# Performance work log

Measured on AMD Instinct MI355X. Metric: run time of the kernel, lower is better.

The kernel has to match this reference:

```python
import jax, jax.numpy as jnp
import numpy as np

B, T, D = 2, 2048, 2048
H, HD = 16, 128          # n_heads, head_dim = d_out // n_heads
DC, DR = 512, 64         # latent dim d_c, rope dim d_R


def _rope(x):
    """RoPE over last dim (even), positions along axis -2. x: [..., T, Dr]."""
    half = x.shape[-1] // 2
    t = x.shape[-2]
    inv_freq = 1.0 / (10000.0 ** (jnp.arange(half, dtype=jnp.float32) / half))
    freqs = jnp.arange(t, dtype=jnp.float32)[:, None] * inv_freq[None, :]  # [T, half]
    sin, cos = jnp.sin(freqs), jnp.cos(freqs)
    x1, x2 = x[..., :half], x[..., half:]
    # stack pairs on a new last axis then flatten -> interleaved layout,
    # matching torch.stack((...), dim=-1) followed by implicit flatten
    rot = jnp.stack([x1 * cos - x2 * sin, x1 * sin + x2 * cos], axis=-1)
    return rot.reshape(x.shape[:-1] + (2 * half,))


def setup_inputs() -> dict:
    key = jax.random.key(0)
    ks = jax.random.split(key, 10)
    s = 0.02  # init scale
    return {
        "x":     jax.random.normal(ks[0], (B, T, D), dtype=jnp.float32),
        "W_DKV": jax.random.normal(ks[1], (D, DC), dtype=jnp.float32) * s,
        "W_DQ":  jax.random.normal(ks[2], (D, DC), dtype=jnp.float32) * s,
        "W_UK":  jax.random.normal(ks[3], (DC, D), dtype=jnp.float32) * s,
        "W_UV":  jax.random.normal(ks[4], (DC, D), dtype=jnp.float32) * s,
        "W_UQ":  jax.random.normal(ks[5], (DC, D), dtype=jnp.float32) * s,
        "W_KR":  jax.random.normal(ks[6], (D, DR), dtype=jnp.float32) * s,
        "W_QR":  jax.random.normal(ks[7], (DC, H * DR), dtype=jnp.float32) * s,
        "W_O":   jax.random.normal(ks[8], (D, D), dtype=jnp.float32) * s,
        "b_O":   jax.random.normal(ks[9], (D,), dtype=jnp.float32) * s,
    }


def reference(x, W_DKV, W_DQ, W_UK, W_UV, W_UQ, W_KR, W_QR, W_O, b_O):
    b, t, d = x.shape
    # latent KV compression and up-projection
    c_kv = x @ W_DKV                                        # [B,T,d_c]
    K = (c_kv @ W_UK).reshape(b, t, H, HD).transpose(0, 2, 1, 3)  # [B,H,T,hd]
    V = (c_kv @ W_UV).reshape(b, t, H, HD).transpose(0, 2, 1, 3)
    # latent Q compression and up-projection
    c_q = x @ W_DQ                                          # [B,T,d_c]
    Q = (c_q @ W_UQ).reshape(b, t, H, HD).transpose(0, 2, 1, 3)
    # decoupled RoPE channels: shared rotary key per token, per-head rotary query
    k_R = _rope(x @ W_KR)[:, None, :, :]                    # [B,1,T,d_R]
    k_R = jnp.broadcast_to(k_R, (b, H, t, DR))
    q_R = (c_q @ W_QR).reshape(b, t, H, DR).transpose(0, 2, 1, 3)  # [B,H,T,d_R]
    q_R = _rope(q_R)
    # concat content + rotary channels
    Kf = jnp.concatenate([K, k_R], axis=-1)                 # [B,H,T,hd+d_R]
    Qf = jnp.concatenate([Q, q_R], axis=-1)
    scale = 1.0 / jnp.sqrt(jnp.float32(HD + DR))
    scores = jnp.einsum('bhqd,bhkd->bhqk', Qf, Kf) * scale  # [B,H,T,T]
    attn = jax.nn.softmax(scores, axis=-1)                  # dropout is identity (p=0 / eval)
    ctx = jnp.einsum('bhqk,bhkd->bhqd', attn, V)            # [B,H,T,hd]
    ctx = ctx.transpose(0, 2, 1, 3).reshape(b, t, d)
    return ctx @ W_O + b_O
```

## Files before the change

### kernel.cpp

```cpp
#include <hip/hip_runtime.h>
#include <hip/hip_bf16.h>

typedef __attribute__((ext_vector_type(8))) short short8;
typedef __attribute__((ext_vector_type(4))) short s4_t;
typedef __attribute__((ext_vector_type(4))) float f32x4;
typedef __attribute__((ext_vector_type(16))) float f32x16;
typedef __attribute__((ext_vector_type(2))) unsigned uint2v;
typedef __hip_bfloat16 bf16;

#define NB 2
#define NT 2048
#define NDIM 2048
#define NH 16
#define NHD 128
#define NDC 512
#define NDR 64

__device__ __forceinline__ void gl_lds16(const bf16* g, bf16* l){
  __builtin_amdgcn_global_load_lds(
      (const __attribute__((address_space(1))) void*)(const void*)g,
      (__attribute__((address_space(3))) void*)(void*)l, 16, 0, 0);
}

__global__ __launch_bounds__(256) void cvt_kernel(const float* __restrict__ src, bf16* __restrict__ dst){
  int i = (blockIdx.x*256 + threadIdx.x)*4;
  float4 v = *(const float4*)(src + i);
  dst[i+0] = __float2bfloat16(v.x);
  dst[i+1] = __float2bfloat16(v.y);
  dst[i+2] = __float2bfloat16(v.z);
  dst[i+3] = __float2bfloat16(v.w);
}

struct TAll {
  const float* src[8];
  bf16* dst[8];
  int K[8];
  int N[8];
  int cum[9];
};
__global__ __launch_bounds__(256) void tconv_all(TAll a){
  __shared__ float tile[32][33];
  int bid = blockIdx.x;
  int i = 0;
  #pragma unroll
  for (int j=0;j<8;j++) if (bid >= a.cum[j+1]) i = j+1;
  const float* W = a.src[i];
  bf16* Wt = a.dst[i];
  int K = a.K[i], N = a.N[i];
  int tl = bid - a.cum[i];
  int ntx = N >> 5;
  int n0 = (tl % ntx)*32, k0 = (tl / ntx)*32;
  int tx = threadIdx.x & 31, ty = threadIdx.x >> 5;
  #pragma unroll
  for (int j=0;j<32;j+=8) tile[ty+j][tx] = W[(size_t)(k0+ty+j)*N + n0 + tx];
  __syncthreads();
  #pragma unroll
  for (int j=0;j<32;j+=8) Wt[(size_t)(n0+ty+j)*K + k0 + tx] = __float2bfloat16(tile[tx][ty+j]);
}

template<int MODE>
__global__ __launch_bounds__(256,3) void gemm_bt(const bf16* __restrict__ A,
    const bf16* __restrict__ Bt, bf16* __restrict__ C, float* __restrict__ Cf,
    const float* __restrict__ bias, int M, int N, int K, int lda, int Tq, int Dpad, float mult)
{
  __shared__ bf16 As[128*64];
  __shared__ bf16 Bs[128*64];
  const int m0 = blockIdx.x*128, n0 = blockIdx.y*128;
  const int t = threadIdx.x, lane = t&63, w = t>>6;
  const int wr = w>>1, wc = w&1;
  const int l15 = lane&15, lg = lane>>4;
  const int wbase = t & 192;

  f32x4 acc[4][4];
  #pragma unroll
  for (int mi=0;mi<4;mi++)
    #pragma unroll
    for (int nj=0;nj<4;nj++) acc[mi][nj] = (f32x4){0.f,0.f,0.f,0.f};

  for (int k0=0;k0<K;k0+=64){
    __syncthreads();
    #pragma unroll
    for (int j=0;j<4;j++){
      int c = j*256 + t;
      int r = c>>3, cc = (c&7)*8;
      gl_lds16(A + (size_t)(m0+r)*lda + k0 + cc, As + (size_t)(j*256 + wbase)*8);
      int bn = n0 + r; if (bn > N-1) bn = N-1;
      gl_lds16(Bt + (size_t)bn*K + k0 + cc, Bs + (size_t)(j*256 + wbase)*8);
    }
    __syncthreads();
    #pragma unroll
    for (int kk=0;kk<2;kk++){
      short8 af[4], bfv[4];
      #pragma unroll
      for (int mi=0;mi<4;mi++) af[mi] = *(const short8*)&As[(wr*64+mi*16+l15)*64 + kk*32+lg*8];
      #pragma unroll
      for (int nj=0;nj<4;nj++) bfv[nj] = *(const short8*)&Bs[(wc*64+nj*16+l15)*64 + kk*32+lg*8];
      #pragma unroll
      for (int mi=0;mi<4;mi++)
        #pragma unroll
        for (int nj=0;nj<4;nj++)
          acc[mi][nj] = __builtin_amdgcn_mfma_f32_16x16x32_bf16(af[mi], bfv[nj], acc[mi][nj], 0,0,0);
    }
  }

  #pragma unroll
  for (int mi=0;mi<4;mi++){
    #pragma unroll
    for (int nj=0;nj<4;nj++){
      f32x4 v = acc[mi][nj];
      int gr0 = m0 + wr*64 + mi*16 + lg*4;
      int gc  = n0 + wc*64 + nj*16 + l15;
      if constexpr (MODE==0){
        if (gc < N){
          #pragma unroll
          for (int r2=0;r2<4;r2++) C[(size_t)(gr0+r2)*N + gc] = __float2bfloat16(v[r2]*mult);
        }
      } else if constexpr (MODE==1){
        int bidx = m0 / Tq;
        int hq = gc >> 7, dl = gc & 127;
        int Hn = N >> 7;
        size_t base = ((size_t)bidx*Hn + hq)*(size_t)Tq;
        int tl0 = (m0 % Tq) + wr*64 + mi*16 + lg*4;
        #pragma unroll
        for (int r2=0;r2<4;r2++) C[(base + tl0 + r2)*Dpad + dl] = __float2bfloat16(v[r2]*mult);
      } else if constexpr (MODE==3){
        int bidx = gr0 >> 11;
        int tl0 = gr0 & 2047;
        int hq = gc >> 7, dl = gc & 127;
        s4_t pk;
        #pragma unroll
        for (int r2=0;r2<4;r2++){
          union { bf16 b; unsigned short u; } cvu;
          cvu.b = __float2bfloat16(v[r2]*mult);
          pk[r2] = (short)cvu.u;
        }
        *(s4_t*)&C[(((size_t)bidx*NH + hq)*NHD + dl)*NT + tl0] = pk;
      } else {
        float bb = bias[gc];
        #pragma unroll
        for (int r2=0;r2<4;r2++) Cf[(size_t)(gr0+r2)*N + gc] = v[r2]*mult + bb;
      }
    }
  }
}

__global__ __launch_bounds__(128) void rope_kernel(const bf16* __restrict__ krp,
    const bf16* __restrict__ qrp, bf16* __restrict__ Kf, bf16* __restrict__ Qf)
{
  int bt = blockIdx.x*2 + (threadIdx.x>>6);
  int d = threadIdx.x & 63;
  int b = bt >> 11, tpos = bt & 2047;
  int i = d >> 1;
  const float scale = 0.07216878364870323f;
  float inv = __expf(-(float)i * 0.2878231366242557f);
  float fr = (float)tpos * inv;
  float sn, cs;
  sincosf(fr, &sn, &cs);

  float x1 = __bfloat162float(krp[(size_t)bt*1088 + i]);
  float x2 = __bfloat162float(krp[(size_t)bt*1088 + 32 + i]);
  float kv = (d&1) ? (x1*sn + x2*cs) : (x1*cs - x2*sn);
  bf16 kvb = __float2bfloat16(kv);
  size_t base = ((size_t)b*NH*NT + tpos)*192;
  #pragma unroll
  for (int h=0;h<NH;h++) Kf[base + (size_t)h*NT*192 + 128 + d] = kvb;

  #pragma unroll
  for (int h=0;h<NH;h++){
    float y1 = __bfloat162float(qrp[bt*1024 + h*64 + i]);
    float y2 = __bfloat162float(qrp[bt*1024 + h*64 + 32 + i]);
    float qv = (d&1) ? (y1*sn + y2*cs) : (y1*cs - y2*sn);
    Qf[base + (size_t)h*NT*192 + 128 + d] = __float2bfloat16(qv*scale);
  }
}

static __device__ inline void plswap(unsigned &a, unsigned &b){
  uint2v r = __builtin_amdgcn_permlane32_swap(a, b, false, false);
  a = r[0]; b = r[1];
}
static __device__ inline unsigned cvtpk(float lo, float hi){
  unsigned u;
  asm("v_cvt_pk_bf16_f32 %0, %1, %2" : "=v"(u) : "v"(lo), "v"(hi));
  return u;
}

__global__ __launch_bounds__(256,2) void attn_kernel(const bf16* __restrict__ Qf,
    const bf16* __restrict__ Kf, const bf16* __restrict__ Vt, bf16* __restrict__ ctx)
{
  __shared__ __align__(16) char smem[40960];
  char* KsB  = smem;
  char* VTsB = smem + 24576;

  const int lin = blockIdx.x;
  const int swz = (lin & 7)*64 + (lin >> 3);
  const int qt = swz & 15, bh = swz >> 4;
  const int b = bh >> 4, h = bh & 15;
  const int q0 = qt * 128;
  const int t = threadIdx.x, lane = t&63, w = t>>6;
  const int l31 = lane&31, hi = lane>>5;
  const int rsw = (l31&7)<<4;
  const int hib = hi*16;

  const bf16* Qp  = Qf + ((size_t)bh*NT + q0)*192;
  const bf16* Kp  = Kf + (size_t)bh*NT*192;
  const bf16* Vtp = Vt + (size_t)bh*NHD*NT;

  short8 qf[12];
  #pragma unroll
  for (int kk=0;kk<12;kk++)
    qf[kk] = *(const short8*)(Qp + (size_t)(w*32 + l31)*192 + kk*16 + hi*8);

  f32x16 o[4];
  #pragma unroll
  for (int Dt=0;Dt<4;Dt++)
    #pragma unroll
    for (int r=0;r<16;r++) o[Dt][r] = 0.f;
  float mrun = -1e30f, lrun = 0.f;

  short8 kst[6], vst[4];
  auto load_tile = [&](int kt){
    const bf16* Ksrc = Kp + (size_t)kt*64*192;
    #pragma unroll
    for (int j=0;j<6;j++) kst[j] = *(const short8*)(Ksrc + (j*256+t)*8);
    #pragma unroll
    for (int j=0;j<4;j++){
      int c = j*256 + t;
      vst[j] = *(const short8*)(Vtp + (size_t)(c>>3)*NT + kt*64 + (c&7)*8);
    }
  };
  load_tile(0);

  for (int kt=0; kt<NT/64; kt++){
    __syncthreads();
    #pragma unroll
    for (int j=0;j<6;j++){
      int c = j*256 + t;
      int r = c/24, cb = (c%24)*16;
      *(short8*)(KsB + r*384 + (cb ^ ((r&7)<<4))) = kst[j];
    }
    #pragma unroll
    for (int j=0;j<4;j++){
      int c = j*256 + t;
      int r = c>>3, cb = (c&7)*16;
      *(short8*)(VTsB + r*128 + (cb ^ ((r&7)<<4))) = vst[j];
    }
    __syncthreads();
    if (kt+1 < NT/64) load_tile(kt+1);

    f32x16 sa[2];
    #pragma unroll
    for (int Mt=0;Mt<2;Mt++)
      #pragma unroll
      for (int r=0;r<16;r++) sa[Mt][r] = 0.f;
    __builtin_amdgcn_s_setprio(1);
    #pragma unroll
    for (int kk=0;kk<12;kk++){
      int cb = kk*32 + hib;
      short8 kf0 = *(const short8*)(KsB + (size_t)l31*384        + ((cb) ^ rsw));
      short8 kf1 = *(const short8*)(KsB + (size_t)(l31+32)*384   + ((cb) ^ rsw));
      sa[0] = __builtin_amdgcn_mfma_f32_32x32x16_bf16(kf0, qf[kk], sa[0], 0,0,0);
      sa[1] = __builtin_amdgcn_mfma_f32_32x32x16_bf16(kf1, qf[kk], sa[1], 0,0,0);
    }
    __builtin_amdgcn_s_setprio(0);

    float mx[8];
    #pragma unroll
    for (int i2=0;i2<8;i2++)
      mx[i2] = fmaxf(fmaxf(sa[0][2*i2], sa[0][2*i2+1]), fmaxf(sa[1][2*i2], sa[1][2*i2+1]));
    float tm = fmaxf(fmaxf(fmaxf(mx[0],mx[1]),fmaxf(mx[2],mx[3])),
                     fmaxf(fmaxf(mx[4],mx[5]),fmaxf(mx[6],mx[7])));
    tm = fmaxf(tm, __shfl_xor(tm, 32));

    if (__any(tm > mrun + 8.f)){
      float mn = fmaxf(mrun, tm);
      float alpha = __expf(mrun - mn);
      mrun = mn;
      lrun *= alpha;
      #pragma unroll
      for (int Dt=0;Dt<4;Dt++)
        #pragma unroll
        for (int r=0;r<16;r++) o[Dt][r] *= alpha;
    }

    #pragma unroll
    for (int Mt=0;Mt<2;Mt++)
      #pragma unroll
      for (int r=0;r<16;r++) sa[Mt][r] = __expf(sa[Mt][r] - mrun);
    float sm[8];
    #pragma unroll
    for (int i2=0;i2<8;i2++)
      sm[i2] = (sa[0][2*i2] + sa[0][2*i2+1]) + (sa[1][2*i2] + sa[1][2*i2+1]);
    float rs = ((sm[0]+sm[1])+(sm[2]+sm[3])) + ((sm[4]+sm[5])+(sm[6]+sm[7]));
    rs += __shfl_xor(rs, 32);
    lrun += rs;

    short8 pf[4];
    #pragma unroll
    for (int Mt=0;Mt<2;Mt++){
      unsigned u[8];
      #pragma unroll
      for (int p8=0;p8<8;p8++) u[p8] = cvtpk(sa[Mt][2*p8], sa[Mt][2*p8+1]);
      plswap(u[0], u[2]); plswap(u[1], u[3]);
      plswap(u[4], u[6]); plswap(u[5], u[7]);
      union { unsigned du[4]; short8 s8; } f0, f1;
      f0.du[0]=u[0]; f0.du[1]=u[1]; f0.du[2]=u[2]; f0.du[3]=u[3];
      f1.du[0]=u[4]; f1.du[1]=u[5]; f1.du[2]=u[6]; f1.du[3]=u[7];
      pf[2*Mt+0] = f0.s8;
      pf[2*Mt+1] = f1.s8;
    }

    __builtin_amdgcn_s_setprio(1);
    #pragma unroll
    for (int kw=0;kw<4;kw++){
      int cb = kw*32 + hib;
      #pragma unroll
      for (int Dt=0;Dt<4;Dt++){
        short8 vf = *(const short8*)(VTsB + (size_t)(Dt*32 + l31)*128 + ((cb) ^ rsw));
        o[Dt] = __builtin_amdgcn_mfma_f32_32x32x16_bf16(vf, pf[kw], o[Dt], 0,0,0);
      }
    }
    __builtin_amdgcn_s_setprio(0);
  }

  __syncthreads();
  float il = 1.0f / lrun;
  bf16* Es = (bf16*)smem;
  const int EROW = 136;
  const int ebase = w*32*EROW;
  #pragma unroll
  for (int Dt=0;Dt<4;Dt++)
    #pragma unroll
    for (int r=0;r<16;r++){
      int d = Dt*32 + (r&3) + 8*(r>>2) + 4*hi;
      Es[ebase + l31*EROW + d] = __float2bfloat16(o[Dt][r]*il);
    }
  __syncthreads();
  int q = lane>>1, halfd = lane&1;
  size_t gq = q0 + w*32 + q;
  size_t obase = (((size_t)b*NT + gq)*NH + h)*NHD + halfd*64;
  #pragma unroll
  for (int pp=0;pp<8;pp++)
    *(short8*)&ctx[obase + pp*8] = *(short8*)&Es[ebase + q*EROW + halfd*64 + pp*8];
}

extern "C" void kernel_launch(void* const* d_in, const int* in_sizes, int n_in,
                              void* d_out, int out_size, void* d_ws, size_t ws_size,
                              hipStream_t stream)
{
  const float* x     = (const float*)d_in[0];
  const float* W_DKV = (const float*)d_in[1];
  const float* W_DQ  = (const float*)d_in[2];
  const float* W_UK  = (const float*)d_in[3];
  const float* W_UV  = (const float*)d_in[4];
  const float* W_UQ  = (const float*)d_in[5];
  const float* W_KR  = (const float*)d_in[6];
  const float* W_QR  = (const float*)d_in[7];
  const float* W_O   = (const float*)d_in[8];
  const float* b_O   = (const float*)d_in[9];

  const float scale = 0.07216878364870323f;

  char* ws = (char*)d_ws;
  bf16* xb    = (bf16*)(ws + 0);
  bf16* wcomb = (bf16*)(ws + 16777216);
  bf16* wuk   = (bf16*)(ws + 21233664);
  bf16* wuv   = (bf16*)(ws + 23330816);
  bf16* wuq   = (bf16*)(ws + 25427968);
  bf16* wqr   = (bf16*)(ws + 27525120);
  bf16* wo    = (bf16*)(ws + 28573696);
  bf16* comb  = (bf16*)(ws + 36962304);
  bf16* qrp   = (bf16*)(ws + 45875200);
  bf16* Qf    = (bf16*)(ws + 54263808);
  bf16* Kf    = (bf16*)(ws + 79429632);
  bf16* vt    = (bf16*)(ws + 104595456);
  bf16* ctxb  = (bf16*)(ws + 121372672);

  bf16* ckv = comb;
  bf16* cq  = comb + 512;
  bf16* krp = comb + 1024;

  cvt_kernel<<<8192,256,0,stream>>>(x, xb);

  TAll ta;
  ta.src[0]=W_DKV; ta.dst[0]=wcomb;             ta.K[0]=2048; ta.N[0]=512;
  ta.src[1]=W_DQ;  ta.dst[1]=wcomb + 512*2048;  ta.K[1]=2048; ta.N[1]=512;
  ta.src[2]=W_KR;  ta.dst[2]=wcomb + 1024*2048; ta.K[2]=2048; ta.N[2]=64;
  ta.src[3]=W_UK;  ta.dst[3]=wuk;               ta.K[3]=512;  ta.N[3]=2048;
  ta.src[4]=W_UV;  ta.dst[4]=wuv;               ta.K[4]=512;  ta.N[4]=2048;
  ta.src[5]=W_UQ;  ta.dst[5]=wuq;               ta.K[5]=512;  ta.N[5]=2048;
  ta.src[6]=W_QR;  ta.dst[6]=wqr;               ta.K[6]=512;  ta.N[6]=1024;
  ta.src[7]=W_O;   ta.dst[7]=wo;                ta.K[7]=2048; ta.N[7]=2048;
  ta.cum[0]=0;
  for (int i=0;i<8;i++) ta.cum[i+1] = ta.cum[i] + (ta.N[i]/32)*(ta.K[i]/32);
  tconv_all<<<ta.cum[8],256,0,stream>>>(ta);

  gemm_bt<0><<<dim3(32,9), 256,0,stream>>>(xb, wcomb, comb, nullptr, nullptr, 4096, 1088, 2048, 2048, 1, 0, 1.0f);

  gemm_bt<1><<<dim3(32,16),256,0,stream>>>(ckv, wuk, Kf, nullptr, nullptr, 4096, 2048, 512, 1088, 2048, 192, 1.0f);
  gemm_bt<3><<<dim3(32,16),256,0,stream>>>(ckv, wuv, vt, nullptr, nullptr, 4096, 2048, 512, 1088, 2048, 128, 1.0f);
  gemm_bt<1><<<dim3(32,16),256,0,stream>>>(cq,  wuq, Qf, nullptr, nullptr, 4096, 2048, 512, 1088, 2048, 192, scale);
  gemm_bt<0><<<dim3(32,8), 256,0,stream>>>(cq,  wqr, qrp, nullptr, nullptr, 4096, 1024, 512, 1088, 1, 0, 1.0f);

  rope_kernel<<<2048,128,0,stream>>>(krp, qrp, Kf, Qf);
  attn_kernel<<<512,256,0,stream>>>(Qf, Kf, vt, ctxb);
  gemm_bt<2><<<dim3(32,16),256,0,stream>>>(ctxb, wo, nullptr, (float*)d_out, b_O, 4096, 2048, 2048, 2048, 1, 0, 1.0f);
}
```

Baseline: 286.2 us.

## Double-buffer attention K/V tiles in LDS and merge up-projection GEMM launches

The attention kernel now keeps two LDS buffers for K and V^T tiles. This removes one of the two barriers per key tile, and the next tile's global loads are issued before the barrier, so staging can overlap compute. LDS per block doubles to 80 KB, which could limit occupancy. The K/V up-projections and the Q/Q-rope up-projections are also merged into two wider GEMM launches with split epilogues. The merged launches assume the paired transposed weight buffers are contiguous in memory.

```diff
diff --git a/kernel.cpp b/kernel.cpp
--- a/kernel.cpp
+++ b/kernel.cpp
@@ -60,8 +60,9 @@
 
 template<int MODE>
 __global__ __launch_bounds__(256,3) void gemm_bt(const bf16* __restrict__ A,
-    const bf16* __restrict__ Bt, bf16* __restrict__ C, float* __restrict__ Cf,
-    const float* __restrict__ bias, int M, int N, int K, int lda, int Tq, int Dpad, float mult)
+    const bf16* __restrict__ Bt, bf16* __restrict__ C, bf16* __restrict__ C2,
+    float* __restrict__ Cf, const float* __restrict__ bias,
+    int M, int N, int K, int lda, float mult)
 {
   __shared__ bf16 As[128*64];
   __shared__ bf16 Bs[128*64];
@@ -115,30 +116,42 @@
           #pragma unroll
           for (int r2=0;r2<4;r2++) C[(size_t)(gr0+r2)*N + gc] = __float2bfloat16(v[r2]*mult);
         }
-      } else if constexpr (MODE==1){
-        int bidx = m0 / Tq;
-        int hq = gc >> 7, dl = gc & 127;
-        int Hn = N >> 7;
-        size_t base = ((size_t)bidx*Hn + hq)*(size_t)Tq;
-        int tl0 = (m0 % Tq) + wr*64 + mi*16 + lg*4;
-        #pragma unroll
-        for (int r2=0;r2<4;r2++) C[(base + tl0 + r2)*Dpad + dl] = __float2bfloat16(v[r2]*mult);
-      } else if constexpr (MODE==3){
-        int bidx = gr0 >> 11;
-        int tl0 = gr0 & 2047;
-        int hq = gc >> 7, dl = gc & 127;
-        s4_t pk;
-        #pragma unroll
-        for (int r2=0;r2<4;r2++){
-          union { bf16 b; unsigned short u; } cvu;
-          cvu.b = __float2bfloat16(v[r2]*mult);
-          pk[r2] = (short)cvu.u;
-        }
-        *(s4_t*)&C[(((size_t)bidx*NH + hq)*NHD + dl)*NT + tl0] = pk;
-      } else {
+      } else if constexpr (MODE==2){
         float bb = bias[gc];
         #pragma unroll
         for (int r2=0;r2<4;r2++) Cf[(size_t)(gr0+r2)*N + gc] = v[r2]*mult + bb;
+      } else if constexpr (MODE==4){
+        int bidx = m0 >> 11;
+        int tl0 = (m0 & 2047) + wr*64 + mi*16 + lg*4;
+        if (gc < 2048){
+          int hq = gc >> 7, dl = gc & 127;
+          size_t base = ((size_t)bidx*NH + hq)*(size_t)NT;
+          #pragma unroll
+          for (int r2=0;r2<4;r2++) C[(base + tl0 + r2)*192 + dl] = __float2bfloat16(v[r2]);
+        } else {
+          int g2 = gc - 2048;
+          int hq = g2 >> 7, dl = g2 & 127;
+          s4_t pk;
+          #pragma unroll
+          for (int r2=0;r2<4;r2++){
+            union { bf16 b; unsigned short u; } cvu;
+            cvu.b = __float2bfloat16(v[r2]);
+            pk[r2] = (short)cvu.u;
+          }
+          *(s4_t*)&C2[(((size_t)bidx*NH + hq)*NHD + dl)*NT + tl0] = pk;
+        }
+      } else {
+        if (gc < 2048){
+          int bidx = m0 >> 11;
+          int tl0 = (m0 & 2047) + wr*64 + mi*16 + lg*4;
+          int hq = gc >> 7, dl = gc & 127;
+          size_t base = ((size_t)bidx*NH + hq)*(size_t)NT;
+          #pragma unroll
+          for (int r2=0;r2<4;r2++) C[(base + tl0 + r2)*192 + dl] = __float2bfloat16(v[r2]*mult);
+        } else {
+          #pragma unroll
+          for (int r2=0;r2<4;r2++) C2[(size_t)(gr0+r2)*1024 + (gc-2048)] = __float2bfloat16(v[r2]);
+        }
       }
     }
   }
@@ -187,9 +200,7 @@
 __global__ __launch_bounds__(256,2) void attn_kernel(const bf16* __restrict__ Qf,
     const bf16* __restrict__ Kf, const bf16* __restrict__ Vt, bf16* __restrict__ ctx)
 {
-  __shared__ __align__(16) char smem[40960];
-  char* KsB  = smem;
-  char* VTsB = smem + 24576;
+  __shared__ __align__(16) char smem[81920];
 
   const int lin = blockIdx.x;
   const int swz = (lin & 7)*64 + (lin >> 3);
@@ -231,7 +242,8 @@
   load_tile(0);
 
   for (int kt=0; kt<NT/64; kt++){
-    __syncthreads();
+    char* KsB  = smem + (kt&1)*40960;
+    char* VTsB = KsB + 24576;
     #pragma unroll
     for (int j=0;j<6;j++){
       int c = j*256 + t;
@@ -244,8 +256,8 @@
       int r = c>>3, cb = (c&7)*16;
       *(short8*)(VTsB + r*128 + (cb ^ ((r&7)<<4))) = vst[j];
     }
+    if (kt+1 < NT/64) load_tile(kt+1);
     __syncthreads();
-    if (kt+1 < NT/64) load_tile(kt+1);
 
     f32x16 sa[2];
     #pragma unroll
@@ -394,14 +406,12 @@
   for (int i=0;i<8;i++) ta.cum[i+1] = ta.cum[i] + (ta.N[i]/32)*(ta.K[i]/32);
   tconv_all<<<ta.cum[8],256,0,stream>>>(ta);
 
-  gemm_bt<0><<<dim3(32,9), 256,0,stream>>>(xb, wcomb, comb, nullptr, nullptr, 4096, 1088, 2048, 2048, 1, 0, 1.0f);
-
-  gemm_bt<1><<<dim3(32,16),256,0,stream>>>(ckv, wuk, Kf, nullptr, nullptr, 4096, 2048, 512, 1088, 2048, 192, 1.0f);
-  gemm_bt<3><<<dim3(32,16),256,0,stream>>>(ckv, wuv, vt, nullptr, nullptr, 4096, 2048, 512, 1088, 2048, 128, 1.0f);
-  gemm_bt<1><<<dim3(32,16),256,0,stream>>>(cq,  wuq, Qf, nullptr, nullptr, 4096, 2048, 512, 1088, 2048, 192, scale);
-  gemm_bt<0><<<dim3(32,8), 256,0,stream>>>(cq,  wqr, qrp, nullptr, nullptr, 4096, 1024, 512, 1088, 1, 0, 1.0f);
+  gemm_bt<0><<<dim3(32,9), 256,0,stream>>>(xb, wcomb, comb, nullptr, nullptr, nullptr, 4096, 1088, 2048, 2048, 1.0f);
+
+  gemm_bt<4><<<dim3(32,32),256,0,stream>>>(ckv, wuk, Kf, vt, nullptr, nullptr, 4096, 4096, 512, 1088, 1.0f);
+  gemm_bt<5><<<dim3(32,24),256,0,stream>>>(cq, wuq, Qf, qrp, nullptr, nullptr, 4096, 3072, 512, 1088, scale);
 
   rope_kernel<<<2048,128,0,stream>>>(krp, qrp, Kf, Qf);
   attn_kernel<<<512,256,0,stream>>>(Qf, Kf, vt, ctxb);
-  gemm_bt<2><<<dim3(32,16),256,0,stream>>>(ctxb, wo, nullptr, (float*)d_out, b_O, 4096, 2048, 2048, 2048, 1, 0, 1.0f);
-}
+  gemm_bt<2><<<dim3(32,16),256,0,stream>>>(ctxb, wo, nullptr, nullptr, (float*)d_out, b_O, 4096, 2048, 2048, 2048, 1.0f);
+}
```

Result: faster. 272.3 us (-4.9%).
